# Performance work log

Hardware: AMD Instinct MI355X
Metric: run time of the kernel (lower is better)

## Reference

```python
import jax, jax.numpy as jnp
import numpy as np

DIM = 512
HEADS = 8
HD = DIM // HEADS

def _rotate_half(t):
    t1, t2 = jnp.split(t, 2, axis=-1)
    return jnp.concatenate((-t2, t1), axis=-1)

def _layernorm(x, g, b, eps=1e-5):
    mu = jnp.mean(x, axis=-1, keepdims=True)
    var = jnp.var(x, axis=-1, keepdims=True)
    return (x - mu) * jax.lax.rsqrt(var + eps) * g + b

def setup_inputs() -> dict:
    key = jax.random.key(0)
    ks = jax.random.split(key, 12)
    B, S = 4, 2048
    x = jax.random.normal(ks[0], (B, S, DIM), dtype=jnp.float32)
    rope_cos = jax.random.uniform(ks[1], (1, S, 1, HD), dtype=jnp.float32)
    rope_sin = jax.random.uniform(ks[2], (1, S, 1, HD), dtype=jnp.float32)
    sd = 1.0 / np.sqrt(DIM)
    params = {
        'norm1_g': jnp.ones((DIM,), jnp.float32),
        'norm1_b': jnp.zeros((DIM,), jnp.float32),
        'norm2_g': jnp.ones((DIM,), jnp.float32),
        'norm2_b': jnp.zeros((DIM,), jnp.float32),
        'w_qkv': jax.random.uniform(ks[3], (DIM, 3 * DIM), jnp.float32, -sd, sd),
        'b_qkv': jax.random.uniform(ks[4], (3 * DIM,), jnp.float32, -sd, sd),
        'w_proj': jax.random.uniform(ks[5], (DIM, DIM), jnp.float32, -sd, sd),
        'b_proj': jax.random.uniform(ks[6], (DIM,), jnp.float32, -sd, sd),
        'w_fc1': jax.random.uniform(ks[7], (DIM, 4 * DIM), jnp.float32, -sd, sd),
        'b_fc1': jax.random.uniform(ks[8], (4 * DIM,), jnp.float32, -sd, sd),
        'w_fc2': jax.random.uniform(ks[9], (4 * DIM, DIM), jnp.float32, -1.0 / np.sqrt(4 * DIM), 1.0 / np.sqrt(4 * DIM)),
        'b_fc2': jax.random.uniform(ks[10], (DIM,), jnp.float32, -1.0 / np.sqrt(4 * DIM), 1.0 / np.sqrt(4 * DIM)),
    }
    return {'x': x, 'rope_cos': rope_cos, 'rope_sin': rope_sin, **params}

def reference(x, rope_cos, rope_sin, norm1_g, norm1_b, norm2_g, norm2_b,
              w_qkv, b_qkv, w_proj, b_proj, w_fc1, b_fc1, w_fc2, b_fc2):
    B, S, D = x.shape
    scale = 1.0 / np.sqrt(HD)
    shortcut = x
    h = _layernorm(x, norm1_g, norm1_b)
    qkv = (h @ w_qkv + b_qkv).reshape(B, S, 3, HEADS, HD)
    q, k, v = qkv[:, :, 0], qkv[:, :, 1], qkv[:, :, 2]  # [B,S,H,hd]
    q = q * rope_cos + _rotate_half(q) * rope_sin
    k = k * rope_cos + _rotate_half(k) * rope_sin
    # attention over heads: scores [B,H,S,S]
    attn = jnp.einsum('bqhd,bkhd->bhqk', q, k) * scale
    attn = jax.nn.softmax(attn, axis=-1)
    o = jnp.einsum('bhqk,bkhd->bqhd', attn, v).reshape(B, S, D)
    o = o @ w_proj + b_proj
    x = shortcut + o  # dropout is identity in eval
    h2 = _layernorm(x, norm2_g, norm2_b)
    mlp = jax.nn.gelu(h2 @ w_fc1 + b_fc1, approximate=False) @ w_fc2 + b_fc2
    return x + mlp
```

## Files before the change

kernel.cpp:

```cpp
#include <hip/hip_runtime.h>
#include <cstdint>
#include <cstddef>

typedef unsigned short u16;
typedef unsigned int   u32;
typedef __bf16 bf16x8 __attribute__((ext_vector_type(8)));
typedef float  f32x4  __attribute__((ext_vector_type(4)));

#define BS   8192
#define DIMM 512
#define NH   8
#define HD   64
#define SEQ  2048
#define DFF  2048
#define NQKV 1536

#define GLD16(g, l) __builtin_amdgcn_global_load_lds( \
    (__attribute__((address_space(1))) const void*)(g), \
    (__attribute__((address_space(3))) void*)(l), 16, 0, 0)

#define SBAR   __builtin_amdgcn_s_barrier()
#define VMCNT4 asm volatile("s_waitcnt vmcnt(4)" ::: "memory")
#define VMCNT0 asm volatile("s_waitcnt vmcnt(0)" ::: "memory")
#define LGKM0  asm volatile("s_waitcnt lgkmcnt(0)" ::: "memory")

__device__ __forceinline__ float b2f(u16 s) {
  u32 u = ((u32)s) << 16;
  float f; __builtin_memcpy(&f, &u, 4); return f;
}
__device__ __forceinline__ u16 f2b(float f) {
  u32 u; __builtin_memcpy(&u, &f, 4);
  u += 0x7fffu + ((u >> 16) & 1u);
  return (u16)(u >> 16);
}
__device__ __forceinline__ u16 f2b_rtz(float f) {
  u32 u; __builtin_memcpy(&u, &f, 4);
  return (u16)(u >> 16);
}

#define SZ_QKV (DIMM * NQKV)
#define SZ_PRJ (DIMM * DIMM)
#define SZ_F1  (DIMM * DFF)
#define SZ_F2  (DFF * DIMM)
__global__ __launch_bounds__(256) void transpose_all_k(
    const float* __restrict__ w_qkv, const float* __restrict__ w_prj,
    const float* __restrict__ w_f1,  const float* __restrict__ w_f2,
    u16* __restrict__ o_qkv, u16* __restrict__ o_prj,
    u16* __restrict__ o_f1,  u16* __restrict__ o_f2) {
  int idx = blockIdx.x * 256 + threadIdx.x;
  const float* W; u16* O; int Kd, Nd, off;
  if (idx < SZ_QKV)                         { W = w_qkv; O = o_qkv; Kd = DIMM; Nd = NQKV; off = idx; }
  else if (idx < SZ_QKV + SZ_PRJ)           { W = w_prj; O = o_prj; Kd = DIMM; Nd = DIMM; off = idx - SZ_QKV; }
  else if (idx < SZ_QKV + SZ_PRJ + SZ_F1)   { W = w_f1;  O = o_f1;  Kd = DIMM; Nd = DFF;  off = idx - SZ_QKV - SZ_PRJ; }
  else                                      { W = w_f2;  O = o_f2;  Kd = DFF;  Nd = DIMM; off = idx - SZ_QKV - SZ_PRJ - SZ_F1; }
  int n = off / Kd, k = off - n * Kd;
  O[off] = f2b(W[(size_t)k * Nd + n]);
}

__global__ __launch_bounds__(256) void ln_f32b_k(const float* __restrict__ X,
    const float* __restrict__ G, const float* __restrict__ Bb, u16* __restrict__ out) {
  int w = threadIdx.x >> 6, lane = threadIdx.x & 63;
  size_t row = (size_t)blockIdx.x * 4 + w;
  const float* xr = X + row * DIMM;
  float v[8];
  *(float4*)&v[0] = *(const float4*)(xr + lane * 8);
  *(float4*)&v[4] = *(const float4*)(xr + lane * 8 + 4);
  float s = 0.f, s2 = 0.f;
#pragma unroll
  for (int j = 0; j < 8; j++) { s += v[j]; s2 += v[j] * v[j]; }
#pragma unroll
  for (int m = 1; m < 64; m <<= 1) { s += __shfl_xor(s, m); s2 += __shfl_xor(s2, m); }
  float mu = s * (1.f / DIMM);
  float rsd = rsqrtf(s2 * (1.f / DIMM) - mu * mu + 1e-5f);
  float g[8], bb[8];
  *(float4*)&g[0]  = *(const float4*)(G + lane * 8);
  *(float4*)&g[4]  = *(const float4*)(G + lane * 8 + 4);
  *(float4*)&bb[0] = *(const float4*)(Bb + lane * 8);
  *(float4*)&bb[4] = *(const float4*)(Bb + lane * 8 + 4);
  uint4 ov; u16* os = (u16*)&ov;
#pragma unroll
  for (int j = 0; j < 8; j++) os[j] = f2b((v[j] - mu) * rsd * g[j] + bb[j]);
  *(uint4*)(out + row * DIMM + lane * 8) = ov;
}

template <int EPI, int TM, int TN, int BK>
__global__ __launch_bounds__(256) void gemm_bt(const u16* __restrict__ A,
    const u16* __restrict__ BT, const float* __restrict__ bias,
    void* __restrict__ Cout, const float* __restrict__ resid, int N, int Kd) {
  constexpr int CPR  = BK / 8;
  constexpr int CPRB = (BK == 64) ? 3 : 2;
  constexpr int RS   = (BK == 64) ? 0 : 1;
  constexpr int KK   = BK / 32;
  constexpr int WROWS = (TN == 128) ? TM / 2 : TM / 4;
  constexpr int MT   = WROWS / 16;
  constexpr int ALOOP = TM * CPR / 256;
  constexpr int BLOOP = TN * CPR / 256;
  __shared__ __align__(16) u16 a_s[2][TM * BK];
  __shared__ __align__(16) u16 b_s[2][TN * BK];
  int t = threadIdx.x, lane = t & 63, w = t >> 6;
  int l15 = lane & 15, quad = lane >> 4;
  int gx = gridDim.x;
  int lid = blockIdx.x + gx * blockIdx.y;
  int per = (gx * gridDim.y) >> 3;
  int nid = (lid & 7) * per + (lid >> 3);
  int bx = nid % gx, by = nid / gx;
  int m0 = by * TM, n0 = bx * TN;
  int wm = (TN == 128) ? (w >> 1) * WROWS : w * WROWS;
  int wn = (TN == 128) ? (w & 1) * 64 : 0;
  f32x4 z4 = {0.f, 0.f, 0.f, 0.f};
  f32x4 acc[MT][4];
#pragma unroll
  for (int i = 0; i < MT; i++)
#pragma unroll
    for (int j = 0; j < 4; j++) acc[i][j] = z4;

#define GSTAGE(buf, ts) do {                                                  \
    int k0_ = (ts) * BK;                                                      \
    _Pragma("unroll")                                                         \
    for (int i = 0; i < ALOOP; i++) {                                         \
      int c_ = t + i * 256;                                                   \
      int row_ = c_ >> CPRB, pos_ = c_ & (CPR - 1);                           \
      int ch_ = (pos_ ^ (row_ >> RS)) & (CPR - 1);                            \
      GLD16(A + (size_t)(m0 + row_) * Kd + k0_ + ch_ * 8, &a_s[buf][c_ * 8]); \
    }                                                                         \
    _Pragma("unroll")                                                         \
    for (int i = 0; i < BLOOP; i++) {                                         \
      int c_ = t + i * 256;                                                   \
      int row_ = c_ >> CPRB, pos_ = c_ & (CPR - 1);                           \
      int ch_ = (pos_ ^ (row_ >> RS)) & (CPR - 1);                            \
      GLD16(BT + (size_t)(n0 + row_) * Kd + k0_ + ch_ * 8, &b_s[buf][c_ * 8]);\
    }                                                                         \
  } while (0)

#define GFRAG(buf) do {                                                       \
    _Pragma("unroll")                                                         \
    for (int mt = 0; mt < MT; mt++) {                                         \
      _Pragma("unroll")                                                       \
      for (int kk = 0; kk < KK; kk++) {                                       \
        int row_ = wm + mt * 16 + l15;                                        \
        int pos_ = ((kk * 4 + quad) ^ (row_ >> RS)) & (CPR - 1);              \
        af[mt][kk] = *(const bf16x8*)&a_s[buf][row_ * BK + pos_ * 8];         \
      }                                                                       \
    }                                                                         \
    _Pragma("unroll")                                                         \
    for (int nt = 0; nt < 4; nt++) {                                          \
      _Pragma("unroll")                                                       \
      for (int kk = 0; kk < KK; kk++) {                                       \
        int row_ = wn + nt * 16 + l15;                                        \
        int pos_ = ((kk * 4 + quad) ^ (row_ >> RS)) & (CPR - 1);              \
        bfm[nt][kk] = *(const bf16x8*)&b_s[buf][row_ * BK + pos_ * 8];        \
      }                                                                       \
    }                                                                         \
  } while (0)

#define GMFMA() do {                                                          \
    _Pragma("unroll")                                                         \
    for (int kk = 0; kk < KK; kk++)                                           \
      _Pragma("unroll")                                                       \
      for (int mt = 0; mt < MT; mt++)                                         \
        _Pragma("unroll")                                                     \
        for (int nt = 0; nt < 4; nt++)                                        \
          acc[mt][nt] = __builtin_amdgcn_mfma_f32_16x16x32_bf16(              \
              af[mt][kk], bfm[nt][kk], acc[mt][nt], 0, 0, 0);                 \
  } while (0)

  bf16x8 af[MT][KK], bfm[4][KK];
  GSTAGE(0, 0);
  GSTAGE(1, 1);
  VMCNT4;
  SBAR;
  int nsteps = Kd / BK;
  for (int ts = 0; ts < nsteps; ts += 2) {
    GFRAG(0);
    LGKM0;
    SBAR;
    if (ts + 2 < nsteps) {
      GSTAGE(0, ts + 2);
      GMFMA();
      VMCNT4;
    } else {
      GMFMA();
      VMCNT0;
    }
    SBAR;
    GFRAG(1);
    LGKM0;
    SBAR;
    if (ts + 3 < nsteps) {
      GSTAGE(1, ts + 3);
      GMFMA();
      VMCNT4;
    } else {
      GMFMA();
      VMCNT0;
    }
    SBAR;
  }
#undef GSTAGE
#undef GFRAG
#undef GMFMA

#pragma unroll
  for (int nt = 0; nt < 4; nt++) {
    int col = n0 + wn + nt * 16 + l15;
    float bv = bias[col];
#pragma unroll
    for (int mt = 0; mt < MT; mt++) {
#pragma unroll
      for (int r = 0; r < 4; r++) {
        int rw = m0 + wm + mt * 16 + quad * 4 + r;
        float v = acc[mt][nt][r] + bv;
        size_t off = (size_t)rw * N + col;
        if (EPI == 0) {
          ((float*)Cout)[off] = v;
        } else if (EPI == 1) {
          ((float*)Cout)[off] = v + resid[off];
        } else if (EPI == 2) {
          ((u16*)Cout)[off] = f2b(0.5f * v * (1.f + erff(v * 0.70710678118654752f)));
        } else {
          ((u16*)Cout)[off] = f2b(v);
        }
      }
    }
  }
}

#define QSCALE 0.18033688f
__global__ __launch_bounds__(256) void rope_k(const u16* __restrict__ qkv,
    const float* __restrict__ C, const float* __restrict__ Sn,
    u16* __restrict__ Qo, u16* __restrict__ Ko, u16* __restrict__ Vo) {
  int idx = blockIdx.x * 256 + threadIdx.x;
  int row = idx / 192;
  int cn = idx - row * 192;
  int n0 = cn * 8;
  int comp = n0 >> 9;
  int hh = (n0 >> 6) & 7;
  int d0 = n0 & 63;
  int b = row >> 11, s = row & 2047;
  const u16* src = qkv + (size_t)row * NQKV;
  uint4 val = *(const uint4*)(src + n0);
  u16* vs = (u16*)&val;
  size_t oo = ((size_t)((b << 3) + hh) * SEQ + s) * HD + d0;
  if (comp == 2) { *(uint4*)(Vo + oo) = val; return; }
  uint4 pv = *(const uint4*)(src + (n0 ^ 32));
  u16* ps = (u16*)&pv;
  float cv[8], sv[8];
  *(float4*)&cv[0] = *(const float4*)(C + s * HD + d0);
  *(float4*)&cv[4] = *(const float4*)(C + s * HD + d0 + 4);
  *(float4*)&sv[0] = *(const float4*)(Sn + s * HD + d0);
  *(float4*)&sv[4] = *(const float4*)(Sn + s * HD + d0 + 4);
  float sgn = (d0 & 32) ? 1.f : -1.f;
  float sc = (comp == 0) ? QSCALE : 1.f;
  uint4 ov; u16* os = (u16*)&ov;
#pragma unroll
  for (int j = 0; j < 8; j++)
    os[j] = f2b(sc * (b2f(vs[j]) * cv[j] + sgn * b2f(ps[j]) * sv[j]));
  *(uint4*)((comp == 0 ? Qo : Ko) + oo) = ov;
}

__global__ __launch_bounds__(256) void vtrans_k(const u16* __restrict__ V,
                                                u16* __restrict__ Vt) {
  __shared__ u16 ld[64 * 72];
  int t = threadIdx.x;
  int bh = blockIdx.x >> 5;
  int s0 = (blockIdx.x & 31) * 64;
  const u16* src = V + (size_t)bh * SEQ * HD + (size_t)s0 * HD;
  u16* dst = Vt + (size_t)bh * SEQ * HD;
#pragma unroll
  for (int i = 0; i < 2; i++) {
    int c = t + i * 256, s = c >> 3, cp = c & 7;
    *(uint4*)&ld[s * 72 + ((cp ^ (s >> 3)) << 3)] =
        *(const uint4*)(src + (size_t)s * HD + cp * 8);
  }
  __syncthreads();
#pragma unroll
  for (int i = 0; i < 2; i++) {
    int c = t + i * 256, d = c >> 3, sc = c & 7;
    uint4 ov; u16* os = (u16*)&ov;
#pragma unroll
    for (int j = 0; j < 8; j++) {
      int s = sc * 8 + j;
      os[j] = ld[s * 72 + (((d >> 3) ^ (s >> 3)) << 3) + (d & 7)];
    }
    *(uint4*)(dst + (size_t)d * SEQ + s0 + sc * 8) = ov;
  }
}

__global__ __launch_bounds__(512) void attn_flash_k(const u16* __restrict__ Qg,
    const u16* __restrict__ Kg, const u16* __restrict__ Vtg, u16* __restrict__ Og) {
  __shared__ u16 q_s[128 * 72];
  __shared__ u16 k_s[64 * 72];
  __shared__ u16 vt_s[64 * 72];
  int t = threadIdx.x, lane = t & 63, w = t >> 6;
  int l15 = lane & 15, quad = lane >> 4;
  int lid = blockIdx.x;
  int nid = (lid & 7) * 64 + (lid >> 3);
  int bh = nid >> 4;
  int qt0 = (nid & 15) * 128;
  int b = bh >> 3, h = bh & 7;
  const u16* Qp = Qg + (size_t)bh * SEQ * HD;
  const u16* Kp = Kg + (size_t)bh * SEQ * HD;
  const u16* Vp = Vtg + (size_t)bh * SEQ * HD;
  int row = t >> 3, ch = t & 7;

  int sW = (w * 4 + quad) & 7;
  int pcol[4];
#pragma unroll
  for (int n = 0; n < 4; n++)
    pcol[n] = (((n * 2 + (l15 >> 3)) ^ sW) << 3) + (l15 & 7);
  int sR = (w * 4 + (l15 >> 2)) & 7;
  int pch[2];
#pragma unroll
  for (int kk = 0; kk < 2; kk++)
    pch[kk] = ((kk * 4 + quad) ^ sR) << 3;

#pragma unroll
  for (int i = 0; i < 2; i++) {
    int c = t + i * 512, qr = c >> 3, qc = c & 7;
    *(uint4*)&q_s[qr * 72 + qc * 8] = *(const uint4*)(Qp + (size_t)(qt0 + qr) * HD + qc * 8);
  }
  uint4 kr = *(const uint4*)(Kp + (size_t)row * HD + ch * 8);
  uint4 vr = *(const uint4*)(Vp + (size_t)row * SEQ + ch * 8);
  __syncthreads();
  bf16x8 qa[2];
  qa[0] = *(const bf16x8*)&q_s[(w * 16 + l15) * 72 + quad * 8];
  qa[1] = *(const bf16x8*)&q_s[(w * 16 + l15) * 72 + 32 + quad * 8];
  u16* p_s = q_s;
  f32x4 z4 = {0.f, 0.f, 0.f, 0.f};
  f32x4 of[4];
#pragma unroll
  for (int n = 0; n < 4; n++) of[n] = z4;
  float lrun[4] = {};

  for (int kt = 0; kt < SEQ; kt += 64) {
    __syncthreads();
    *(uint4*)&k_s[row * 72 + ch * 8] = kr;
    *(uint4*)&vt_s[row * 72 + ch * 8] = vr;
    __syncthreads();
    if (kt + 64 < SEQ) {
      kr = *(const uint4*)(Kp + (size_t)(kt + 64 + row) * HD + ch * 8);
      vr = *(const uint4*)(Vp + (size_t)row * SEQ + kt + 64 + ch * 8);
    }
    f32x4 sf[4];
#pragma unroll
    for (int n = 0; n < 4; n++) sf[n] = z4;
    __builtin_amdgcn_s_setprio(1);
#pragma unroll
    for (int kk = 0; kk < 2; kk++)
#pragma unroll
      for (int n = 0; n < 4; n++) {
        bf16x8 kb = *(const bf16x8*)&k_s[(n * 16 + l15) * 72 + kk * 32 + quad * 8];
        sf[n] = __builtin_amdgcn_mfma_f32_16x16x32_bf16(qa[kk], kb, sf[n], 0, 0, 0);
      }
    __builtin_amdgcn_s_setprio(0);
#pragma unroll
    for (int r = 0; r < 4; r++) {
      int prow = (w * 16 + quad * 4 + r) * 72;
#pragma unroll
      for (int n = 0; n < 4; n++) {
        float pp = exp2f(sf[n][r]);
        lrun[r] += pp;
        p_s[prow + pcol[n]] = f2b_rtz(pp);
      }
    }
    __builtin_amdgcn_s_setprio(1);
#pragma unroll
    for (int kk = 0; kk < 2; kk++) {
      bf16x8 pa = *(const bf16x8*)&p_s[(w * 16 + l15) * 72 + pch[kk]];
#pragma unroll
      for (int n = 0; n < 4; n++) {
        bf16x8 vb = *(const bf16x8*)&vt_s[(n * 16 + l15) * 72 + kk * 32 + quad * 8];
        of[n] = __builtin_amdgcn_mfma_f32_16x16x32_bf16(pa, vb, of[n], 0, 0, 0);
      }
    }
    __builtin_amdgcn_s_setprio(0);
  }
#pragma unroll
  for (int r = 0; r < 4; r++) {
    float l = lrun[r];
#pragma unroll
    for (int m = 1; m < 16; m <<= 1) l += __shfl_xor(l, m);
    float inv = 1.f / l;
    size_t orow = (size_t)(b * SEQ + qt0 + w * 16 + quad * 4 + r);
#pragma unroll
    for (int n = 0; n < 4; n++)
      Og[orow * DIMM + h * HD + n * 16 + l15] = f2b(of[n][r] * inv);
  }
}

extern "C" void kernel_launch(void* const* d_in, const int* in_sizes, int n_in,
                              void* d_out, int out_size, void* d_ws, size_t ws_size,
                              hipStream_t stream) {
  const float* x    = (const float*)d_in[0];
  const float* rc   = (const float*)d_in[1];
  const float* rsn  = (const float*)d_in[2];
  const float* n1g  = (const float*)d_in[3];
  const float* n1b  = (const float*)d_in[4];
  const float* n2g  = (const float*)d_in[5];
  const float* n2b  = (const float*)d_in[6];
  const float* wqkv = (const float*)d_in[7];
  const float* bqkv = (const float*)d_in[8];
  const float* wprj = (const float*)d_in[9];
  const float* bprj = (const float*)d_in[10];
  const float* wf1  = (const float*)d_in[11];
  const float* bf1  = (const float*)d_in[12];
  const float* wf2  = (const float*)d_in[13];
  const float* bf2  = (const float*)d_in[14];

  char* p = (char*)d_ws;
  u16*   wqkvT = (u16*)p;
  u16*   wprjT = (u16*)(p + (2u  << 20));
  u16*   wf1T  = (u16*)(p + (3u  << 20));
  u16*   wf2T  = (u16*)(p + (5u  << 20));
  u16*   h1    = (u16*)(p + (8u  << 20));
  u16*   qkvb  = (u16*)(p + (16u << 20));
  u16*   Vt    = (u16*)(p + (40u << 20));
  u16*   Qb    = (u16*)(p + (64u << 20));
  u16*   Kb    = (u16*)(p + (72u << 20));
  u16*   Vb    = (u16*)(p + (80u << 20));
  float* x2    = (float*)(p + (88u << 20));
  u16*   ob    = h1;
  u16*   h2    = h1;
  u16*   mid   = qkvb;

  transpose_all_k<<<dim3((SZ_QKV + SZ_PRJ + SZ_F1 + SZ_F2) / 256), 256, 0, stream>>>(
      wqkv, wprj, wf1, wf2, wqkvT, wprjT, wf1T, wf2T);

  ln_f32b_k<<<dim3(BS / 4), 256, 0, stream>>>(x, n1g, n1b, h1);

  gemm_bt<3, 128, 128, 32><<<dim3(NQKV / 128, BS / 128), 256, 0, stream>>>(h1, wqkvT, bqkv, qkvb, nullptr, NQKV, DIMM);

  rope_k<<<dim3(BS * NQKV / 8 / 256), 256, 0, stream>>>(qkvb, rc, rsn, Qb, Kb, Vb);

  vtrans_k<<<dim3(32 * (SEQ / 64)), 256, 0, stream>>>(Vb, Vt);

  attn_flash_k<<<dim3(32 * (SEQ / 128)), 512, 0, stream>>>(Qb, Kb, Vt, ob);

  gemm_bt<1, 64, 64, 64><<<dim3(DIMM / 64, BS / 64), 256, 0, stream>>>(ob, wprjT, bprj, x2, x, DIMM, DIMM);

  ln_f32b_k<<<dim3(BS / 4), 256, 0, stream>>>(x2, n2g, n2b, h2);

  gemm_bt<2, 128, 128, 32><<<dim3(DFF / 128, BS / 128), 256, 0, stream>>>(h2, wf1T, bf1, mid, nullptr, DFF, DIMM);

  gemm_bt<1, 64, 64, 64><<<dim3(DIMM / 64, BS / 64), 256, 0, stream>>>(mid, wf2T, bf2, (float*)d_out, x2, DIMM, DFF);
}
```

Before: 340.4 us.

## Split attention over two key halves and combine partial results

```diff
diff --git a/kernel.cpp b/kernel.cpp
--- a/kernel.cpp
+++ b/kernel.cpp
@@ -287,16 +287,19 @@
 }
 
 __global__ __launch_bounds__(512) void attn_flash_k(const u16* __restrict__ Qg,
-    const u16* __restrict__ Kg, const u16* __restrict__ Vtg, u16* __restrict__ Og) {
+    const u16* __restrict__ Kg, const u16* __restrict__ Vtg,
+    float* __restrict__ Op, float* __restrict__ Lp) {
   __shared__ u16 q_s[128 * 72];
   __shared__ u16 k_s[64 * 72];
   __shared__ u16 vt_s[64 * 72];
   int t = threadIdx.x, lane = t & 63, w = t >> 6;
   int l15 = lane & 15, quad = lane >> 4;
   int lid = blockIdx.x;
-  int nid = (lid & 7) * 64 + (lid >> 3);
-  int bh = nid >> 4;
+  int nid = (lid & 7) * 128 + (lid >> 3);
+  int bhh = nid >> 4;
+  int bh = bhh >> 1, half = bhh & 1;
   int qt0 = (nid & 15) * 128;
+  int kt0 = half << 10;
   int b = bh >> 3, h = bh & 7;
   const u16* Qp = Qg + (size_t)bh * SEQ * HD;
   const u16* Kp = Kg + (size_t)bh * SEQ * HD;
@@ -319,8 +322,8 @@
     int c = t + i * 512, qr = c >> 3, qc = c & 7;
     *(uint4*)&q_s[qr * 72 + qc * 8] = *(const uint4*)(Qp + (size_t)(qt0 + qr) * HD + qc * 8);
   }
-  uint4 kr = *(const uint4*)(Kp + (size_t)row * HD + ch * 8);
-  uint4 vr = *(const uint4*)(Vp + (size_t)row * SEQ + ch * 8);
+  uint4 kr = *(const uint4*)(Kp + (size_t)(kt0 + row) * HD + ch * 8);
+  uint4 vr = *(const uint4*)(Vp + (size_t)row * SEQ + kt0 + ch * 8);
   __syncthreads();
   bf16x8 qa[2];
   qa[0] = *(const bf16x8*)&q_s[(w * 16 + l15) * 72 + quad * 8];
@@ -332,12 +335,12 @@
   for (int n = 0; n < 4; n++) of[n] = z4;
   float lrun[4] = {};
 
-  for (int kt = 0; kt < SEQ; kt += 64) {
+  for (int kt = kt0; kt < kt0 + 1024; kt += 64) {
     __syncthreads();
     *(uint4*)&k_s[row * 72 + ch * 8] = kr;
     *(uint4*)&vt_s[row * 72 + ch * 8] = vr;
     __syncthreads();
-    if (kt + 64 < SEQ) {
+    if (kt + 64 < kt0 + 1024) {
       kr = *(const uint4*)(Kp + (size_t)(kt + 64 + row) * HD + ch * 8);
       vr = *(const uint4*)(Vp + (size_t)row * SEQ + kt + 64 + ch * 8);
     }
@@ -375,17 +378,43 @@
     }
     __builtin_amdgcn_s_setprio(0);
   }
+  float* Opb = Op + (size_t)half * ((size_t)BS * DIMM);
+  float* Lpb = Lp + (size_t)half * (32 * 2048);
 #pragma unroll
   for (int r = 0; r < 4; r++) {
     float l = lrun[r];
 #pragma unroll
     for (int m = 1; m < 16; m <<= 1) l += __shfl_xor(l, m);
-    float inv = 1.f / l;
-    size_t orow = (size_t)(b * SEQ + qt0 + w * 16 + quad * 4 + r);
+    int s = qt0 + w * 16 + quad * 4 + r;
+    size_t orow = (size_t)b * SEQ + s;
 #pragma unroll
     for (int n = 0; n < 4; n++)
-      Og[orow * DIMM + h * HD + n * 16 + l15] = f2b(of[n][r] * inv);
-  }
+      Opb[orow * DIMM + h * HD + n * 16 + l15] = of[n][r];
+    if (l15 == 0) Lpb[(bh << 11) + s] = l;
+  }
+}
+
+__global__ __launch_bounds__(256) void attn_combine_k(const float* __restrict__ Op,
+    const float* __restrict__ Lp, u16* __restrict__ ob) {
+  int idx = blockIdx.x * 256 + threadIdx.x;
+  size_t off8 = (size_t)idx * 8;
+  int row = (int)(off8 >> 9), col = (int)(off8 & 511);
+  int h = col >> 6;
+  int b = row >> 11, s = row & 2047;
+  int li = (((b << 3) + h) << 11) + s;
+  float inv = 1.f / (Lp[li] + Lp[li + (32 << 11)]);
+  const float* O0 = Op + off8;
+  const float* O1 = Op + (size_t)BS * DIMM + off8;
+  float4 a0 = *(const float4*)(O0);
+  float4 a1 = *(const float4*)(O0 + 4);
+  float4 c0 = *(const float4*)(O1);
+  float4 c1 = *(const float4*)(O1 + 4);
+  uint4 ov; u16* os = (u16*)&ov;
+  os[0] = f2b((a0.x + c0.x) * inv); os[1] = f2b((a0.y + c0.y) * inv);
+  os[2] = f2b((a0.z + c0.z) * inv); os[3] = f2b((a0.w + c0.w) * inv);
+  os[4] = f2b((a1.x + c1.x) * inv); os[5] = f2b((a1.y + c1.y) * inv);
+  os[6] = f2b((a1.z + c1.z) * inv); os[7] = f2b((a1.w + c1.w) * inv);
+  *(uint4*)(ob + off8) = ov;
 }
 
 extern "C" void kernel_launch(void* const* d_in, const int* in_sizes, int n_in,
@@ -414,7 +443,9 @@
   u16*   wf2T  = (u16*)(p + (5u  << 20));
   u16*   h1    = (u16*)(p + (8u  << 20));
   u16*   qkvb  = (u16*)(p + (16u << 20));
-  u16*   Vt    = (u16*)(p + (40u << 20));
+  float* Opart = (float*)(p + (16u << 20));
+  u16*   Vt    = (u16*)(p + (48u << 20));
+  float* Lpart = (float*)(p + (56u << 20));
   u16*   Qb    = (u16*)(p + (64u << 20));
   u16*   Kb    = (u16*)(p + (72u << 20));
   u16*   Vb    = (u16*)(p + (80u << 20));
@@ -434,7 +465,9 @@
 
   vtrans_k<<<dim3(32 * (SEQ / 64)), 256, 0, stream>>>(Vb, Vt);
 
-  attn_flash_k<<<dim3(32 * (SEQ / 128)), 512, 0, stream>>>(Qb, Kb, Vt, ob);
+  attn_flash_k<<<dim3(2 * 32 * (SEQ / 128)), 512, 0, stream>>>(Qb, Kb, Vt, Opart, Lpart);
+
+  attn_combine_k<<<dim3(BS * DIMM / 8 / 256), 256, 0, stream>>>(Opart, Lpart, ob);
 
   gemm_bt<1, 64, 64, 64><<<dim3(DIMM / 64, BS / 64), 256, 0, stream>>>(ob, wprjT, bprj, x2, x, DIMM, DIMM);
 
```

Measured after the change: 345.9 us. No clear change (+1.6%).
